# Kernel optimization log

Hardware: AMD Instinct MI355X
Metric: run time of the kernel (lower is better)

The kernel has to match this reference:

```python
import jax, jax.numpy as jnp
import numpy as np
import math

B, S, IN_DIM = 4, 2048, 512
D, H, L, FF = 256, 4, 4, 2048
HD = D // H
EPS = 1e-5


def _pos_encoding(S, D, dtype=jnp.float32):
    pos = jnp.arange(S, dtype=jnp.float32)[:, None]
    div = jnp.exp(jnp.arange(0, D, 2, dtype=jnp.float32) * (-math.log(10000.0) / D))
    pe = jnp.zeros((S, D), dtype=jnp.float32)
    pe = pe.at[:, 0::2].set(jnp.sin(pos * div))
    pe = pe.at[:, 1::2].set(jnp.cos(pos * div))
    return pe.astype(dtype)


def _layernorm(x, w, b):
    mu = jnp.mean(x, axis=-1, keepdims=True)
    var = jnp.var(x, axis=-1, keepdims=True)
    return (x - mu) * jax.lax.rsqrt(var + EPS) * w + b


def setup_inputs() -> dict:
    key = jax.random.key(0)
    ks = jax.random.split(key, 12)
    sc = 0.02
    inp = {
        "x": jax.random.normal(ks[0], (B, S, IN_DIM), dtype=jnp.float32),
        "W_in": jax.random.normal(ks[1], (D, IN_DIM), dtype=jnp.float32) * sc,
        "b_in": jnp.zeros((D,), dtype=jnp.float32),
        "qkv_w": jax.random.normal(ks[2], (L, 3 * D, D), dtype=jnp.float32) * sc,
        "qkv_b": jnp.zeros((L, 3 * D), dtype=jnp.float32),
        "out_w": jax.random.normal(ks[3], (L, D, D), dtype=jnp.float32) * sc,
        "out_b": jnp.zeros((L, D), dtype=jnp.float32),
        "ln1_w": jnp.ones((L, D), dtype=jnp.float32),
        "ln1_b": jnp.zeros((L, D), dtype=jnp.float32),
        "ff1_w": jax.random.normal(ks[4], (L, FF, D), dtype=jnp.float32) * sc,
        "ff1_b": jnp.zeros((L, FF), dtype=jnp.float32),
        "ff2_w": jax.random.normal(ks[5], (L, D, FF), dtype=jnp.float32) * sc,
        "ff2_b": jnp.zeros((L, D), dtype=jnp.float32),
        "ln2_w": jnp.ones((L, D), dtype=jnp.float32),
        "ln2_b": jnp.zeros((L, D), dtype=jnp.float32),
        "W_fc": jax.random.normal(ks[6], (IN_DIM, D), dtype=jnp.float32) * sc,
        "b_fc": jnp.zeros((IN_DIM,), dtype=jnp.float32),
    }
    return inp


def reference(x, W_in, b_in, qkv_w, qkv_b, out_w, out_b, ln1_w, ln1_b,
              ff1_w, ff1_b, ff2_w, ff2_b, ln2_w, ln2_b, W_fc, b_fc):
    # input projection + positional encoding (dropout=0 / eval)
    h = jnp.einsum('bsi,di->bsd', x, W_in) + b_in
    h = h + _pos_encoding(S, D, h.dtype)[None]

    scale = 1.0 / math.sqrt(HD)
    for l in range(L):
        # --- self-attention (unfused: explicit QK^T + softmax + V) ---
        qkv = jnp.einsum('bsd,ed->bse', h, qkv_w[l]) + qkv_b[l]  # [B,S,3D]
        q, k, v = jnp.split(qkv, 3, axis=-1)
        q = q.reshape(B, S, H, HD).transpose(0, 2, 1, 3)  # [B,H,S,HD]
        k = k.reshape(B, S, H, HD).transpose(0, 2, 1, 3)
        v = v.reshape(B, S, H, HD).transpose(0, 2, 1, 3)
        scores = jnp.einsum('bhqd,bhkd->bhqk', q, k) * scale  # [B,H,S,S]
        attn = jax.nn.softmax(scores, axis=-1)
        ctx = jnp.einsum('bhqk,bhkd->bhqd', attn, v)
        ctx = ctx.transpose(0, 2, 1, 3).reshape(B, S, D)
        sa = jnp.einsum('bsd,ed->bse', ctx, out_w[l]) + out_b[l]
        h = _layernorm(h + sa, ln1_w[l], ln1_b[l])  # post-norm
        # --- feed-forward (relu) ---
        ff = jax.nn.relu(jnp.einsum('bsd,fd->bsf', h, ff1_w[l]) + ff1_b[l])
        ff = jnp.einsum('bsf,df->bsd', ff, ff2_w[l]) + ff2_b[l]
        h = _layernorm(h + ff, ln2_w[l], ln2_b[l])

    # final projection from last time step
    return jnp.einsum('bd,od->bo', h[:, -1, :], W_fc) + b_fc  # [B, IN_DIM]
```

## Files before the change

### kernel.cpp

```cpp
#include <hip/hip_runtime.h>
#include <math.h>

#define S_LEN 2048
#define DMODEL 256
#define NHEAD 4
#define HDIM 64
#define NLAYER 4
#define FFDIM 2048
#define INDIM 512
#define BATCH 4
#define NTOK (BATCH * S_LEN)
#define EPSV 1e-5f
#define KSPLIT 4

typedef __attribute__((ext_vector_type(8))) short frag8;
typedef __attribute__((ext_vector_type(4))) float f32x4v;
typedef unsigned short u16;
typedef unsigned int u32;

__device__ __forceinline__ float pe_val(int s, int d) {
    const float c = 0.035977892f;
    float dv = expf(-(float)(d & ~1) * c);
    float arg = (float)s * dv;
    return (d & 1) ? cosf(arg) : sinf(arg);
}

__device__ __forceinline__ u16 f2bf(float f) {
    union { float f; unsigned u; } v; v.f = f;
    unsigned r = v.u + 0x7fffu + ((v.u >> 16) & 1u);
    return (u16)(r >> 16);
}
__device__ __forceinline__ float bf2f(u16 h) {
    union { u32 u; float f; } v; v.u = (u32)h << 16; return v.f;
}
__device__ __forceinline__ u32 pk2bf(float lo, float hi) {
    union { float f; u32 u; } a, b; a.f = lo; b.f = hi;
    return __builtin_amdgcn_perm(b.u, a.u, 0x07060302u);
}
__device__ __forceinline__ void load_lds16(const u16* g, u16* l) {
    __builtin_amdgcn_global_load_lds(
        (const __attribute__((address_space(1))) unsigned int*)g,
        (__attribute__((address_space(3))) unsigned int*)l, 16, 0, 0);
}

__global__ __launch_bounds__(256) void cvt_all(
    const float* __restrict__ x, const float* __restrict__ W_in,
    const float* __restrict__ qkv_w, const float* __restrict__ out_w,
    const float* __restrict__ ff1_w, const float* __restrict__ ff2_w,
    u16* __restrict__ xb, u16* __restrict__ W_in_b,
    u16* __restrict__ qkv_w_b, u16* __restrict__ out_w_b,
    u16* __restrict__ ff1_w_b, u16* __restrict__ ff2_w_b)
{
    const int i = blockIdx.x * 256 + threadIdx.x;
    const float* src; u16* dst; int base;
    if (i < 1048576)      { src = x;     dst = xb;      base = 0; }
    else if (i < 1081344) { src = W_in;  dst = W_in_b;  base = 1048576; }
    else if (i < 1277952) { src = qkv_w; dst = qkv_w_b; base = 1081344; }
    else if (i < 1343488) { src = out_w; dst = out_w_b; base = 1277952; }
    else if (i < 1867776) { src = ff1_w; dst = ff1_w_b; base = 1343488; }
    else                  { src = ff2_w; dst = ff2_w_b; base = 1867776; }
    const int e = (i - base) * 4;
    const float4 v = *(const float4*)(src + e);
    ushort4 o;
    o.x = f2bf(v.x); o.y = f2bf(v.y); o.z = f2bf(v.z); o.w = f2bf(v.w);
    *(ushort4*)(dst + e) = o;
}

template <int MODE>
__global__ __launch_bounds__(256) void gemm_mfma(
    const u16* __restrict__ A, const u16* __restrict__ W,
    const float* __restrict__ bias, u16* __restrict__ Cb,
    int M, int N, int K)
{
    __shared__ __align__(16) u16 As[128 * 32];
    __shared__ __align__(16) u16 Bs[128 * 32];
    const int t = threadIdx.x;
    const int w = t >> 6, lane = t & 63;
    const int col = lane & 15, quad = lane >> 4;
    const int qx = (quad ^ ((col >> 1) & 3)) * 8;
    const int m0 = blockIdx.x * 128, n0 = blockIdx.y * 128;
    const int wm = (w >> 1) * 64, wn = (w & 1) * 64;

    const int r0 = lane >> 2;
    const int kc = ((lane & 3) ^ ((lane >> 3) & 3)) * 8;
    const u16* pA0 = A + (size_t)(m0 + (w * 2 + 0) * 16 + r0) * K + kc;
    const u16* pA1 = A + (size_t)(m0 + (w * 2 + 1) * 16 + r0) * K + kc;
    const u16* pB0 = W + (size_t)(n0 + (w * 2 + 0) * 16 + r0) * K + kc;
    const u16* pB1 = W + (size_t)(n0 + (w * 2 + 1) * 16 + r0) * K + kc;
    u16* lA0 = As + (w * 2 + 0) * 512;
    u16* lA1 = As + (w * 2 + 1) * 512;
    u16* lB0 = Bs + (w * 2 + 0) * 512;
    u16* lB1 = Bs + (w * 2 + 1) * 512;

    f32x4v acc[4][4];
#pragma unroll
    for (int i = 0; i < 4; ++i)
#pragma unroll
        for (int j = 0; j < 4; ++j) acc[i][j] = (f32x4v){0.f, 0.f, 0.f, 0.f};

    for (int kb = 0; kb < K; kb += 32) {
        __syncthreads();
        load_lds16(pA0 + kb, lA0);
        load_lds16(pA1 + kb, lA1);
        load_lds16(pB0 + kb, lB0);
        load_lds16(pB1 + kb, lB1);
        __syncthreads();

        frag8 a[4], b[4];
#pragma unroll
        for (int i = 0; i < 4; ++i)
            a[i] = *(const frag8*)&As[(wm + i * 16 + col) * 32 + qx];
#pragma unroll
        for (int j = 0; j < 4; ++j)
            b[j] = *(const frag8*)&Bs[(wn + j * 16 + col) * 32 + qx];
#pragma unroll
        for (int i = 0; i < 4; ++i)
#pragma unroll
            for (int j = 0; j < 4; ++j)
                acc[i][j] = __builtin_amdgcn_mfma_f32_16x16x32_bf16(
                    a[i], b[j], acc[i][j], 0, 0, 0);
    }

#pragma unroll
    for (int j = 0; j < 4; ++j) {
        const int cn = n0 + wn + j * 16 + col;
        const float bv = bias[cn];
#pragma unroll
        for (int i = 0; i < 4; ++i) {
            const int cmb = m0 + wm + i * 16 + quad * 4;
#pragma unroll
            for (int r = 0; r < 4; ++r) {
                float v = acc[i][j][r] + bv;
                if (MODE == 2) v = fmaxf(v, 0.f);
                Cb[(size_t)(cmb + r) * N + cn] = f2bf(v);
            }
        }
    }
}

template <int MODE>
__global__ __launch_bounds__(256) void gemm64k(
    const u16* __restrict__ A, const u16* __restrict__ W,
    const float* __restrict__ bias, u16* __restrict__ Cb,
    u16* __restrict__ aux, int M, int N, int K)
{
    __shared__ __align__(16) u16 As[64 * 64];
    __shared__ __align__(16) u16 Bs[64 * 64];
    const int t = threadIdx.x;
    const int w = t >> 6, lane = t & 63;
    const int col = lane & 15, quad = lane >> 4;
    const int px0 = ((quad ^ (col & 7))) * 8;
    const int px1 = px0 ^ 32;
    const int m0 = blockIdx.x * 64, n0 = blockIdx.y * 64;
    const int wm = (w >> 1) * 32, wn = (w & 1) * 32;

    const int sr = lane >> 3;
    const int lc = ((lane & 7) ^ sr) * 8;
    const u16* pA0 = A + (size_t)(m0 + w * 16 + sr) * K + lc;
    const u16* pA1 = A + (size_t)(m0 + w * 16 + 8 + sr) * K + lc;
    const u16* pB0 = W + (size_t)(n0 + w * 16 + sr) * K + lc;
    const u16* pB1 = W + (size_t)(n0 + w * 16 + 8 + sr) * K + lc;
    u16* lA0 = As + (w * 16) * 64;
    u16* lA1 = As + (w * 16 + 8) * 64;
    u16* lB0 = Bs + (w * 16) * 64;
    u16* lB1 = Bs + (w * 16 + 8) * 64;

    f32x4v acc[2][2];
#pragma unroll
    for (int i = 0; i < 2; ++i)
#pragma unroll
        for (int j = 0; j < 2; ++j) acc[i][j] = (f32x4v){0.f, 0.f, 0.f, 0.f};

    for (int kb = 0; kb < K; kb += 64) {
        __syncthreads();
        load_lds16(pA0 + kb, lA0);
        load_lds16(pA1 + kb, lA1);
        load_lds16(pB0 + kb, lB0);
        load_lds16(pB1 + kb, lB1);
        __syncthreads();

#pragma unroll
        for (int kh = 0; kh < 2; ++kh) {
            const int px = kh ? px1 : px0;
            frag8 a[2], b[2];
#pragma unroll
            for (int i = 0; i < 2; ++i)
                a[i] = *(const frag8*)&As[(wm + i * 16 + col) * 64 + px];
#pragma unroll
            for (int j = 0; j < 2; ++j)
                b[j] = *(const frag8*)&Bs[(wn + j * 16 + col) * 64 + px];
#pragma unroll
            for (int i = 0; i < 2; ++i)
#pragma unroll
                for (int j = 0; j < 2; ++j)
                    acc[i][j] = __builtin_amdgcn_mfma_f32_16x16x32_bf16(
                        a[i], b[j], acc[i][j], 0, 0, 0);
        }
    }

#pragma unroll
    for (int j = 0; j < 2; ++j) {
        const int cn = n0 + wn + j * 16 + col;
        const float bv = bias[cn];
#pragma unroll
        for (int i = 0; i < 2; ++i) {
            const int cmb = m0 + wm + i * 16 + quad * 4;
            float vv[4];
#pragma unroll
            for (int r = 0; r < 4; ++r) {
                float v = acc[i][j][r] + bv;
                if (MODE == 1) v += pe_val((cmb + r) & (S_LEN - 1), cn);
                if (MODE == 5) v += bf2f(aux[(size_t)(cmb + r) * N + cn]);
                vv[r] = v;
                Cb[(size_t)(cmb + r) * N + cn] = f2bf(v);
            }
            if (MODE == 4 && cn >= 512) {
                const int dg = cn - 512;
                const int bh = (cmb >> 11) * 4 + (dg >> 6);
                uint2 pk;
                pk.x = ((u32)f2bf(vv[1]) << 16) | f2bf(vv[0]);
                pk.y = ((u32)f2bf(vv[3]) << 16) | f2bf(vv[2]);
                *(uint2*)&aux[((size_t)bh * 64 + (dg & 63)) * S_LEN + (cmb & 2047)] = pk;
            }
        }
    }
}

__global__ __launch_bounds__(256) void attn_part(const u16* __restrict__ qkv,
                                                 const u16* __restrict__ vt,
                                                 u16* __restrict__ Opart,
                                                 float* __restrict__ lpart)
{
    __shared__ __align__(16) u16 Ks0[64 * 32], Ks1[64 * 32];
    __shared__ __align__(16) u16 Vt0[64 * 32], Vt1[64 * 32];
    __shared__ __align__(16) u16 Ps[4][2][2][512];

    const int t = threadIdx.x;
    const int w = t >> 6, lane = t & 63;
    const int col = lane & 15, quad = lane >> 4;
    const int sq = (col >> 1) & 3;
    const int qx = (quad ^ sq) * 8;
    const int bh = blockIdx.x, b = bh >> 2, hh = bh & 3;
    const int qt = blockIdx.y, ks = blockIdx.z;

    const float SCL = 0.125f * 1.44269504f;

    frag8 qf[2][2];
#pragma unroll
    for (int qg = 0; qg < 2; ++qg) {
        const int qrow = qt * 128 + w * 32 + qg * 16 + col;
        const u16* qp = qkv + (size_t)(b * S_LEN + qrow) * 768 + hh * HDIM;
        const frag8 r0 = *(const frag8*)(qp + quad * 8);
        const frag8 r1 = *(const frag8*)(qp + 32 + quad * 8);
#pragma unroll
        for (int e = 0; e < 8; ++e) {
            qf[qg][0][e] = (short)f2bf(bf2f((u16)r0[e]) * SCL);
            qf[qg][1][e] = (short)f2bf(bf2f((u16)r1[e]) * SCL);
        }
    }
    frag8 ones;
#pragma unroll
    for (int e = 0; e < 8; ++e) ones[e] = (short)0x3F80;

    f32x4v Oacc[2][4], lacc[2];
#pragma unroll
    for (int qg = 0; qg < 2; ++qg) {
#pragma unroll
        for (int dt = 0; dt < 4; ++dt) Oacc[qg][dt] = (f32x4v){0.f, 0.f, 0.f, 0.f};
        lacc[qg] = (f32x4v){0.f, 0.f, 0.f, 0.f};
    }

    const int srow = w * 16 + (lane >> 2);
    const int sseg = ((lane & 3) ^ ((lane >> 3) & 3)) * 8;
    const int kb0 = ks * (S_LEN / KSPLIT);
    const u16* kbase = qkv + (size_t)(b * S_LEN + kb0 + srow) * 768
                       + 256 + hh * HDIM + sseg;
    const u16* vbase = vt + ((size_t)bh * 64 + srow) * S_LEN + kb0 + sseg;
    u16* lK0 = Ks0 + w * 512;
    u16* lK1 = Ks1 + w * 512;
    u16* lV0 = Vt0 + w * 512;
    u16* lV1 = Vt1 + w * 512;

    for (int kt = 0; kt < S_LEN / KSPLIT / 64; ++kt) {
        __syncthreads();
        const u16* kp = kbase + (size_t)kt * 64 * 768;
        const u16* vp = vbase + kt * 64;
        load_lds16(kp, lK0);
        load_lds16(kp + 32, lK1);
        load_lds16(vp, lV0);
        load_lds16(vp + 32, lV1);
        __syncthreads();

#pragma unroll
        for (int nt = 0; nt < 4; ++nt) {
            const frag8 k0 = *(const frag8*)&Ks0[(nt * 16 + col) * 32 + qx];
            const frag8 k1 = *(const frag8*)&Ks1[(nt * 16 + col) * 32 + qx];
            const int c = (nt & 1) * 2 + (quad >> 1);
            const int poff = col * 32 + ((c ^ sq) * 8) + (quad & 1) * 4;
#pragma unroll
            for (int qg = 0; qg < 2; ++qg) {
                f32x4v s = (f32x4v){0.f, 0.f, 0.f, 0.f};
                s = __builtin_amdgcn_mfma_f32_16x16x32_bf16(k0, qf[qg][0], s, 0, 0, 0);
                s = __builtin_amdgcn_mfma_f32_16x16x32_bf16(k1, qf[qg][1], s, 0, 0, 0);
                const float p0 = __builtin_amdgcn_exp2f(s[0]);
                const float p1 = __builtin_amdgcn_exp2f(s[1]);
                const float p2 = __builtin_amdgcn_exp2f(s[2]);
                const float p3 = __builtin_amdgcn_exp2f(s[3]);
                uint2 pk;
                pk.x = pk2bf(p0, p1);
                pk.y = pk2bf(p2, p3);
                *(uint2*)&Ps[w][qg][nt >> 1][poff] = pk;
            }
        }

        frag8 pf[2][2];
#pragma unroll
        for (int qg = 0; qg < 2; ++qg) {
            pf[qg][0] = *(const frag8*)&Ps[w][qg][0][col * 32 + qx];
            pf[qg][1] = *(const frag8*)&Ps[w][qg][1][col * 32 + qx];
        }
#pragma unroll
        for (int dt = 0; dt < 4; ++dt) {
            const frag8 v0 = *(const frag8*)&Vt0[(dt * 16 + col) * 32 + qx];
            const frag8 v1 = *(const frag8*)&Vt1[(dt * 16 + col) * 32 + qx];
#pragma unroll
            for (int qg = 0; qg < 2; ++qg) {
                Oacc[qg][dt] = __builtin_amdgcn_mfma_f32_16x16x32_bf16(
                    v0, pf[qg][0], Oacc[qg][dt], 0, 0, 0);
                Oacc[qg][dt] = __builtin_amdgcn_mfma_f32_16x16x32_bf16(
                    v1, pf[qg][1], Oacc[qg][dt], 0, 0, 0);
            }
        }
#pragma unroll
        for (int qg = 0; qg < 2; ++qg) {
            lacc[qg] = __builtin_amdgcn_mfma_f32_16x16x32_bf16(
                ones, pf[qg][0], lacc[qg], 0, 0, 0);
            lacc[qg] = __builtin_amdgcn_mfma_f32_16x16x32_bf16(
                ones, pf[qg][1], lacc[qg], 0, 0, 0);
        }
    }

#pragma unroll
    for (int qg = 0; qg < 2; ++qg) {
        const int qrow = qt * 128 + w * 32 + qg * 16 + col;
        u16* op = Opart + (((size_t)ks * 16 + bh) * S_LEN + qrow) * 64;
#pragma unroll
        for (int dt = 0; dt < 4; ++dt) {
            uint2 pk;
            pk.x = pk2bf(Oacc[qg][dt][0], Oacc[qg][dt][1]);
            pk.y = pk2bf(Oacc[qg][dt][2], Oacc[qg][dt][3]);
            *(uint2*)(op + dt * 16 + quad * 4) = pk;
        }
        if (quad == 0)
            lpart[((size_t)ks * 16 + bh) * S_LEN + qrow] = lacc[qg][0];
    }
}

__global__ __launch_bounds__(256) void attn_combine(const u16* __restrict__ Opart,
                                                    const float* __restrict__ lpart,
                                                    u16* __restrict__ ctx)
{
    const int idx = blockIdx.x * 256 + threadIdx.x;
    const int d4 = idx & 15;
    const int q = (idx >> 4) & (S_LEN - 1);
    const int bh = idx >> 15;
    const int b = bh >> 2, hh = bh & 3;

    float o0 = 0.f, o1 = 0.f, o2 = 0.f, o3 = 0.f, l = 0.f;
#pragma unroll
    for (int ks = 0; ks < KSPLIT; ++ks) {
        const ushort4 po = *(const ushort4*)&Opart[
            (((size_t)ks * 16 + bh) * S_LEN + q) * 64 + d4 * 4];
        o0 += bf2f(po.x); o1 += bf2f(po.y);
        o2 += bf2f(po.z); o3 += bf2f(po.w);
        l += lpart[((size_t)ks * 16 + bh) * S_LEN + q];
    }
    const float inv = 1.f / l;
    ushort4 r;
    r.x = f2bf(o0 * inv); r.y = f2bf(o1 * inv);
    r.z = f2bf(o2 * inv); r.w = f2bf(o3 * inv);
    *(ushort4*)&ctx[((size_t)(b * S_LEN + q)) * DMODEL + hh * HDIM + d4 * 4] = r;
}

__global__ __launch_bounds__(256) void ln_only(u16* __restrict__ hb,
                                               const u16* __restrict__ sab,
                                               const float* __restrict__ w,
                                               const float* __restrict__ b)
{
    const int t = blockIdx.x;
    const int d = threadIdx.x;
    const size_t idx = (size_t)t * DMODEL + d;
    const float x = bf2f(sab[idx]);

    float s = x, s2 = x * x;
#pragma unroll
    for (int off = 32; off; off >>= 1) {
        s += __shfl_down(s, off);
        s2 += __shfl_down(s2, off);
    }
    __shared__ float ls[4], ls2[4];
    __shared__ float mu_s, rs_s;
    const int wid = d >> 6, lane = d & 63;
    if (lane == 0) { ls[wid] = s; ls2[wid] = s2; }
    __syncthreads();
    if (d == 0) {
        const float ts = ls[0] + ls[1] + ls[2] + ls[3];
        const float ts2 = ls2[0] + ls2[1] + ls2[2] + ls2[3];
        const float mu = ts * (1.f / DMODEL);
        const float var = ts2 * (1.f / DMODEL) - mu * mu;
        mu_s = mu;
        rs_s = rsqrtf(var + EPSV);
    }
    __syncthreads();
    hb[idx] = f2bf((x - mu_s) * rs_s * w[d] + b[d]);
}

__global__ __launch_bounds__(256) void final_proj(const u16* __restrict__ hb,
                                                  const float* __restrict__ Wfc,
                                                  const float* __restrict__ bfc,
                                                  float* __restrict__ out)
{
    const int idx = blockIdx.x * 256 + threadIdx.x;
    const int b = idx >> 9;
    const int o = idx & 511;
    const u16* hp = hb + (size_t)(b * S_LEN + S_LEN - 1) * DMODEL;
    const float* wp = Wfc + (size_t)o * DMODEL;
    float s = 0.f;
#pragma unroll 4
    for (int d = 0; d < DMODEL; ++d) s += bf2f(hp[d]) * wp[d];
    out[idx] = s + bfc[o];
}

extern "C" void kernel_launch(void* const* d_in, const int* in_sizes, int n_in,
                              void* d_out, int out_size, void* d_ws, size_t ws_size,
                              hipStream_t stream)
{
    const float* x     = (const float*)d_in[0];
    const float* W_in  = (const float*)d_in[1];
    const float* b_in  = (const float*)d_in[2];
    const float* qkv_w = (const float*)d_in[3];
    const float* qkv_b = (const float*)d_in[4];
    const float* out_w = (const float*)d_in[5];
    const float* out_b = (const float*)d_in[6];
    const float* ln1_w = (const float*)d_in[7];
    const float* ln1_b = (const float*)d_in[8];
    const float* ff1_w = (const float*)d_in[9];
    const float* ff1_b = (const float*)d_in[10];
    const float* ff2_w = (const float*)d_in[11];
    const float* ff2_b = (const float*)d_in[12];
    const float* ln2_w = (const float*)d_in[13];
    const float* ln2_b = (const float*)d_in[14];
    const float* W_fc  = (const float*)d_in[15];
    const float* b_fc  = (const float*)d_in[16];
    float* out = (float*)d_out;

    char* p = (char*)d_ws;
    u16* hb    = (u16*)p;  p += (size_t)NTOK * DMODEL * 2;
    u16* sab   = (u16*)p;  p += (size_t)NTOK * DMODEL * 2;
    u16* xb    = (u16*)p;  p += (size_t)NTOK * INDIM * 2;
    u16* qkvb  = (u16*)p;  p += (size_t)NTOK * 768 * 2;
    u16* ctxb  = (u16*)p;  p += (size_t)NTOK * DMODEL * 2;
    u16* ffb   = (u16*)p;  p += (size_t)NTOK * FFDIM * 2;
    u16* vtb   = (u16*)p;  p += (size_t)16 * 64 * S_LEN * 2;
    u16* W_in_b  = (u16*)p; p += (size_t)131072 * 2;
    u16* qkv_w_b = (u16*)p; p += (size_t)786432 * 2;
    u16* out_w_b = (u16*)p; p += (size_t)262144 * 2;
    u16* ff1_w_b = (u16*)p; p += (size_t)2097152 * 2;
    u16* ff2_w_b = (u16*)p; p += (size_t)2097152 * 2;
    if (ws_size < (size_t)82051072) return;

    u16* Opart = ffb;
    float* lpart = (float*)sab;

    cvt_all<<<9344, 256, 0, stream>>>(x, W_in, qkv_w, out_w, ff1_w, ff2_w,
                                      xb, W_in_b, qkv_w_b, out_w_b, ff1_w_b, ff2_w_b);

    gemm64k<1><<<dim3(NTOK / 64, DMODEL / 64), 256, 0, stream>>>(
        xb, W_in_b, b_in, hb, nullptr, NTOK, DMODEL, INDIM);

    for (int l = 0; l < NLAYER; ++l) {
        gemm64k<4><<<dim3(NTOK / 64, 768 / 64), 256, 0, stream>>>(
            hb, qkv_w_b + (size_t)l * 768 * DMODEL, qkv_b + l * 768,
            qkvb, vtb, NTOK, 768, DMODEL);
        attn_part<<<dim3(BATCH * NHEAD, S_LEN / 128, KSPLIT), 256, 0, stream>>>(
            qkvb, vtb, Opart, lpart);
        attn_combine<<<2048, 256, 0, stream>>>(Opart, lpart, ctxb);
        gemm64k<5><<<dim3(NTOK / 64, DMODEL / 64), 256, 0, stream>>>(
            ctxb, out_w_b + (size_t)l * DMODEL * DMODEL, out_b + l * DMODEL,
            sab, hb, NTOK, DMODEL, DMODEL);
        ln_only<<<NTOK, 256, 0, stream>>>(hb, sab, ln1_w + l * DMODEL, ln1_b + l * DMODEL);
        gemm_mfma<2><<<dim3(NTOK / 128, FFDIM / 128), 256, 0, stream>>>(
            hb, ff1_w_b + (size_t)l * FFDIM * DMODEL, ff1_b + l * FFDIM,
            ffb, NTOK, FFDIM, DMODEL);
        gemm64k<5><<<dim3(NTOK / 64, DMODEL / 64), 256, 0, stream>>>(
            ffb, ff2_w_b + (size_t)l * DMODEL * FFDIM, ff2_b + l * DMODEL,
            sab, hb, NTOK, DMODEL, FFDIM);
        ln_only<<<NTOK, 256, 0, stream>>>(hb, sab, ln2_w + l * DMODEL, ln2_b + l * DMODEL);
    }

    final_proj<<<8, 256, 0, stream>>>(hb, W_fc, b_fc, out);
}
```

Baseline: 566.7 us.

## Double-buffer LDS tiles in GEMM and attention kernels to prefetch next tile

Both the 64x64 GEMM kernel and the split-K attention kernel now keep two LDS buffers for their K/A/B (and V) tiles. The next tile is loaded from global memory into the alternate buffer while the MFMA work runs on the current one. This drops one barrier per loop iteration and aims to hide global-load latency behind compute. In exchange each block uses twice the LDS for those tiles, which may reduce occupancy.

After: 574.3 us. No clear change (+1.4%).

```diff
diff --git a/kernel.cpp b/kernel.cpp
--- a/kernel.cpp
+++ b/kernel.cpp
@@ -144,8 +144,8 @@
     const float* __restrict__ bias, u16* __restrict__ Cb,
     u16* __restrict__ aux, int M, int N, int K)
 {
-    __shared__ __align__(16) u16 As[64 * 64];
-    __shared__ __align__(16) u16 Bs[64 * 64];
+    __shared__ __align__(16) u16 As[2][64 * 64];
+    __shared__ __align__(16) u16 Bs[2][64 * 64];
     const int t = threadIdx.x;
     const int w = t >> 6, lane = t & 63;
     const int col = lane & 15, quad = lane >> 4;
@@ -160,10 +160,7 @@
     const u16* pA1 = A + (size_t)(m0 + w * 16 + 8 + sr) * K + lc;
     const u16* pB0 = W + (size_t)(n0 + w * 16 + sr) * K + lc;
     const u16* pB1 = W + (size_t)(n0 + w * 16 + 8 + sr) * K + lc;
-    u16* lA0 = As + (w * 16) * 64;
-    u16* lA1 = As + (w * 16 + 8) * 64;
-    u16* lB0 = Bs + (w * 16) * 64;
-    u16* lB1 = Bs + (w * 16 + 8) * 64;
+    const int o0 = (w * 16) * 64, o1 = (w * 16 + 8) * 64;
 
     f32x4v acc[2][2];
 #pragma unroll
@@ -171,24 +168,32 @@
 #pragma unroll
         for (int j = 0; j < 2; ++j) acc[i][j] = (f32x4v){0.f, 0.f, 0.f, 0.f};
 
-    for (int kb = 0; kb < K; kb += 64) {
+    load_lds16(pA0, &As[0][o0]);
+    load_lds16(pA1, &As[0][o1]);
+    load_lds16(pB0, &Bs[0][o0]);
+    load_lds16(pB1, &Bs[0][o1]);
+
+    const int NIT = K >> 6;
+    for (int it = 0; it < NIT; ++it) {
+        const int cur = it & 1;
         __syncthreads();
-        load_lds16(pA0 + kb, lA0);
-        load_lds16(pA1 + kb, lA1);
-        load_lds16(pB0 + kb, lB0);
-        load_lds16(pB1 + kb, lB1);
-        __syncthreads();
-
+        if (it + 1 < NIT) {
+            const int kb = (it + 1) << 6;
+            load_lds16(pA0 + kb, &As[cur ^ 1][o0]);
+            load_lds16(pA1 + kb, &As[cur ^ 1][o1]);
+            load_lds16(pB0 + kb, &Bs[cur ^ 1][o0]);
+            load_lds16(pB1 + kb, &Bs[cur ^ 1][o1]);
+        }
 #pragma unroll
         for (int kh = 0; kh < 2; ++kh) {
             const int px = kh ? px1 : px0;
             frag8 a[2], b[2];
 #pragma unroll
             for (int i = 0; i < 2; ++i)
-                a[i] = *(const frag8*)&As[(wm + i * 16 + col) * 64 + px];
+                a[i] = *(const frag8*)&As[cur][(wm + i * 16 + col) * 64 + px];
 #pragma unroll
             for (int j = 0; j < 2; ++j)
-                b[j] = *(const frag8*)&Bs[(wn + j * 16 + col) * 64 + px];
+                b[j] = *(const frag8*)&Bs[cur][(wn + j * 16 + col) * 64 + px];
 #pragma unroll
             for (int i = 0; i < 2; ++i)
 #pragma unroll
@@ -231,8 +236,8 @@
                                                  u16* __restrict__ Opart,
                                                  float* __restrict__ lpart)
 {
-    __shared__ __align__(16) u16 Ks0[64 * 32], Ks1[64 * 32];
-    __shared__ __align__(16) u16 Vt0[64 * 32], Vt1[64 * 32];
+    __shared__ __align__(16) u16 Ks[2][2][64 * 32];
+    __shared__ __align__(16) u16 Vt[2][2][64 * 32];
     __shared__ __align__(16) u16 Ps[4][2][2][512];
 
     const int t = threadIdx.x;
@@ -276,25 +281,29 @@
     const u16* kbase = qkv + (size_t)(b * S_LEN + kb0 + srow) * 768
                        + 256 + hh * HDIM + sseg;
     const u16* vbase = vt + ((size_t)bh * 64 + srow) * S_LEN + kb0 + sseg;
-    u16* lK0 = Ks0 + w * 512;
-    u16* lK1 = Ks1 + w * 512;
-    u16* lV0 = Vt0 + w * 512;
-    u16* lV1 = Vt1 + w * 512;
+    const int so = w * 512;
+
+    load_lds16(kbase, &Ks[0][0][so]);
+    load_lds16(kbase + 32, &Ks[0][1][so]);
+    load_lds16(vbase, &Vt[0][0][so]);
+    load_lds16(vbase + 32, &Vt[0][1][so]);
 
     for (int kt = 0; kt < S_LEN / KSPLIT / 64; ++kt) {
+        const int cur = kt & 1;
         __syncthreads();
-        const u16* kp = kbase + (size_t)kt * 64 * 768;
-        const u16* vp = vbase + kt * 64;
-        load_lds16(kp, lK0);
-        load_lds16(kp + 32, lK1);
-        load_lds16(vp, lV0);
-        load_lds16(vp + 32, lV1);
-        __syncthreads();
+        if (kt + 1 < S_LEN / KSPLIT / 64) {
+            const u16* kp = kbase + (size_t)(kt + 1) * 64 * 768;
+            const u16* vp = vbase + (kt + 1) * 64;
+            load_lds16(kp, &Ks[cur ^ 1][0][so]);
+            load_lds16(kp + 32, &Ks[cur ^ 1][1][so]);
+            load_lds16(vp, &Vt[cur ^ 1][0][so]);
+            load_lds16(vp + 32, &Vt[cur ^ 1][1][so]);
+        }
 
 #pragma unroll
         for (int nt = 0; nt < 4; ++nt) {
-            const frag8 k0 = *(const frag8*)&Ks0[(nt * 16 + col) * 32 + qx];
-            const frag8 k1 = *(const frag8*)&Ks1[(nt * 16 + col) * 32 + qx];
+            const frag8 k0 = *(const frag8*)&Ks[cur][0][(nt * 16 + col) * 32 + qx];
+            const frag8 k1 = *(const frag8*)&Ks[cur][1][(nt * 16 + col) * 32 + qx];
             const int c = (nt & 1) * 2 + (quad >> 1);
             const int poff = col * 32 + ((c ^ sq) * 8) + (quad & 1) * 4;
 #pragma unroll
@@ -321,8 +330,8 @@
         }
 #pragma unroll
         for (int dt = 0; dt < 4; ++dt) {
-            const frag8 v0 = *(const frag8*)&Vt0[(dt * 16 + col) * 32 + qx];
-            const frag8 v1 = *(const frag8*)&Vt1[(dt * 16 + col) * 32 + qx];
+            const frag8 v0 = *(const frag8*)&Vt[cur][0][(dt * 16 + col) * 32 + qx];
+            const frag8 v1 = *(const frag8*)&Vt[cur][1][(dt * 16 + col) * 32 + qx];
 #pragma unroll
             for (int qg = 0; qg < 2; ++qg) {
                 Oacc[qg][dt] = __builtin_amdgcn_mfma_f32_16x16x32_bf16(
```

## Fuse attention split-K combine into out-projection GEMM and double-buffer gemm64k

Applied to the files above, without the earlier changes.

Removes the attn_combine kernel. The out-projection GEMM (new MODE 6) now reduces the KSPLIT partial outputs and normalisers while staging its A tile into LDS, so the ctx buffer is never written or re-read. The gemm64k main loop also gains double-buffered LDS with one barrier per iteration, so loads for the next tile are issued before compute on the current one. This cuts a kernel launch and a round trip to global memory, at the cost of doubled LDS and synchronous register-path loads for the combine inside the GEMM. The lpart buffer moves out of sab into its own workspace region.

Measured after the change: 552.6 us. 1.03x faster.

```diff
diff --git a/kernel.cpp b/kernel.cpp
--- a/kernel.cpp
+++ b/kernel.cpp
@@ -142,10 +142,11 @@
 __global__ __launch_bounds__(256) void gemm64k(
     const u16* __restrict__ A, const u16* __restrict__ W,
     const float* __restrict__ bias, u16* __restrict__ Cb,
-    u16* __restrict__ aux, int M, int N, int K)
-{
-    __shared__ __align__(16) u16 As[64 * 64];
-    __shared__ __align__(16) u16 Bs[64 * 64];
+    u16* __restrict__ aux, const float* __restrict__ lp,
+    int M, int N, int K)
+{
+    __shared__ __align__(16) u16 As[2][64 * 64];
+    __shared__ __align__(16) u16 Bs[2][64 * 64];
     const int t = threadIdx.x;
     const int w = t >> 6, lane = t & 63;
     const int col = lane & 15, quad = lane >> 4;
@@ -160,10 +161,7 @@
     const u16* pA1 = A + (size_t)(m0 + w * 16 + 8 + sr) * K + lc;
     const u16* pB0 = W + (size_t)(n0 + w * 16 + sr) * K + lc;
     const u16* pB1 = W + (size_t)(n0 + w * 16 + 8 + sr) * K + lc;
-    u16* lA0 = As + (w * 16) * 64;
-    u16* lA1 = As + (w * 16 + 8) * 64;
-    u16* lB0 = Bs + (w * 16) * 64;
-    u16* lB1 = Bs + (w * 16 + 8) * 64;
+    const int o0 = (w * 16) * 64, o1 = (w * 16 + 8) * 64;
 
     f32x4v acc[2][2];
 #pragma unroll
@@ -171,24 +169,67 @@
 #pragma unroll
         for (int j = 0; j < 2; ++j) acc[i][j] = (f32x4v){0.f, 0.f, 0.f, 0.f};
 
-    for (int kb = 0; kb < K; kb += 64) {
+    auto stageA = [&](int it, int buf) {
+        if (MODE == 6) {
+            const int hh = it;
+#pragma unroll
+            for (int pos = 0; pos < 2; ++pos) {
+                const int m = m0 + w * 16 + pos * 8 + sr;
+                const int q = m & (S_LEN - 1);
+                const int bh = (m >> 11) * 4 + hh;
+                const size_t basei = (((size_t)bh) * S_LEN + q) * 64 + lc;
+                float l = 0.f;
+                float o[8] = {0.f, 0.f, 0.f, 0.f, 0.f, 0.f, 0.f, 0.f};
+#pragma unroll
+                for (int ksx = 0; ksx < KSPLIT; ++ksx) {
+                    const uint4 pv = *(const uint4*)(A + (size_t)ksx * 16 * S_LEN * 64 + basei);
+                    o[0] += bf2f((u16)(pv.x & 0xffff)); o[1] += bf2f((u16)(pv.x >> 16));
+                    o[2] += bf2f((u16)(pv.y & 0xffff)); o[3] += bf2f((u16)(pv.y >> 16));
+                    o[4] += bf2f((u16)(pv.z & 0xffff)); o[5] += bf2f((u16)(pv.z >> 16));
+                    o[6] += bf2f((u16)(pv.w & 0xffff)); o[7] += bf2f((u16)(pv.w >> 16));
+                    l += lp[((size_t)ksx * 16 + bh) * S_LEN + q];
+                }
+                const float inv = 1.f / l;
+                uint4 pk;
+                pk.x = ((u32)f2bf(o[1] * inv) << 16) | f2bf(o[0] * inv);
+                pk.y = ((u32)f2bf(o[3] * inv) << 16) | f2bf(o[2] * inv);
+                pk.z = ((u32)f2bf(o[5] * inv) << 16) | f2bf(o[4] * inv);
+                pk.w = ((u32)f2bf(o[7] * inv) << 16) | f2bf(o[6] * inv);
+                *(uint4*)&As[buf][(pos ? o1 : o0) + lane * 8] = pk;
+            }
+        } else {
+            const int kb = it << 6;
+            load_lds16(pA0 + kb, &As[buf][o0]);
+            load_lds16(pA1 + kb, &As[buf][o1]);
+        }
+    };
+    auto stageB = [&](int it, int buf) {
+        const int kb = it << 6;
+        load_lds16(pB0 + kb, &Bs[buf][o0]);
+        load_lds16(pB1 + kb, &Bs[buf][o1]);
+    };
+
+    stageA(0, 0);
+    stageB(0, 0);
+
+    const int NIT = K >> 6;
+    for (int it = 0; it < NIT; ++it) {
+        const int cur = it & 1;
         __syncthreads();
-        load_lds16(pA0 + kb, lA0);
-        load_lds16(pA1 + kb, lA1);
-        load_lds16(pB0 + kb, lB0);
-        load_lds16(pB1 + kb, lB1);
-        __syncthreads();
-
+        if (it + 1 < NIT) {
+            stageA(it + 1, cur ^ 1);
+            stageB(it + 1, cur ^ 1);
+        }
 #pragma unroll
         for (int kh = 0; kh < 2; ++kh) {
             const int px = kh ? px1 : px0;
             frag8 a[2], b[2];
 #pragma unroll
             for (int i = 0; i < 2; ++i)
-                a[i] = *(const frag8*)&As[(wm + i * 16 + col) * 64 + px];
+                a[i] = *(const frag8*)&As[cur][(wm + i * 16 + col) * 64 + px];
 #pragma unroll
             for (int j = 0; j < 2; ++j)
-                b[j] = *(const frag8*)&Bs[(wn + j * 16 + col) * 64 + px];
+                b[j] = *(const frag8*)&Bs[cur][(wn + j * 16 + col) * 64 + px];
 #pragma unroll
             for (int i = 0; i < 2; ++i)
 #pragma unroll
@@ -210,7 +251,8 @@
             for (int r = 0; r < 4; ++r) {
                 float v = acc[i][j][r] + bv;
                 if (MODE == 1) v += pe_val((cmb + r) & (S_LEN - 1), cn);
-                if (MODE == 5) v += bf2f(aux[(size_t)(cmb + r) * N + cn]);
+                if (MODE == 5 || MODE == 6)
+                    v += bf2f(aux[(size_t)(cmb + r) * N + cn]);
                 vv[r] = v;
                 Cb[(size_t)(cmb + r) * N + cn] = f2bf(v);
             }
@@ -354,32 +396,6 @@
         if (quad == 0)
             lpart[((size_t)ks * 16 + bh) * S_LEN + qrow] = lacc[qg][0];
     }
-}
-
-__global__ __launch_bounds__(256) void attn_combine(const u16* __restrict__ Opart,
-                                                    const float* __restrict__ lpart,
-                                                    u16* __restrict__ ctx)
-{
-    const int idx = blockIdx.x * 256 + threadIdx.x;
-    const int d4 = idx & 15;
-    const int q = (idx >> 4) & (S_LEN - 1);
-    const int bh = idx >> 15;
-    const int b = bh >> 2, hh = bh & 3;
-
-    float o0 = 0.f, o1 = 0.f, o2 = 0.f, o3 = 0.f, l = 0.f;
-#pragma unroll
-    for (int ks = 0; ks < KSPLIT; ++ks) {
-        const ushort4 po = *(const ushort4*)&Opart[
-            (((size_t)ks * 16 + bh) * S_LEN + q) * 64 + d4 * 4];
-        o0 += bf2f(po.x); o1 += bf2f(po.y);
-        o2 += bf2f(po.z); o3 += bf2f(po.w);
-        l += lpart[((size_t)ks * 16 + bh) * S_LEN + q];
-    }
-    const float inv = 1.f / l;
-    ushort4 r;
-    r.x = f2bf(o0 * inv); r.y = f2bf(o1 * inv);
-    r.z = f2bf(o2 * inv); r.w = f2bf(o3 * inv);
-    *(ushort4*)&ctx[((size_t)(b * S_LEN + q)) * DMODEL + hh * HDIM + d4 * 4] = r;
 }
 
 __global__ __launch_bounds__(256) void ln_only(u16* __restrict__ hb,
@@ -459,42 +475,40 @@
     u16* sab   = (u16*)p;  p += (size_t)NTOK * DMODEL * 2;
     u16* xb    = (u16*)p;  p += (size_t)NTOK * INDIM * 2;
     u16* qkvb  = (u16*)p;  p += (size_t)NTOK * 768 * 2;
-    u16* ctxb  = (u16*)p;  p += (size_t)NTOK * DMODEL * 2;
     u16* ffb   = (u16*)p;  p += (size_t)NTOK * FFDIM * 2;
     u16* vtb   = (u16*)p;  p += (size_t)16 * 64 * S_LEN * 2;
+    float* lpart = (float*)p; p += (size_t)KSPLIT * 16 * S_LEN * 4;
     u16* W_in_b  = (u16*)p; p += (size_t)131072 * 2;
     u16* qkv_w_b = (u16*)p; p += (size_t)786432 * 2;
     u16* out_w_b = (u16*)p; p += (size_t)262144 * 2;
     u16* ff1_w_b = (u16*)p; p += (size_t)2097152 * 2;
     u16* ff2_w_b = (u16*)p; p += (size_t)2097152 * 2;
-    if (ws_size < (size_t)82051072) return;
+    if (ws_size < (size_t)78643200) return;
 
     u16* Opart = ffb;
-    float* lpart = (float*)sab;
 
     cvt_all<<<9344, 256, 0, stream>>>(x, W_in, qkv_w, out_w, ff1_w, ff2_w,
                                       xb, W_in_b, qkv_w_b, out_w_b, ff1_w_b, ff2_w_b);
 
     gemm64k<1><<<dim3(NTOK / 64, DMODEL / 64), 256, 0, stream>>>(
-        xb, W_in_b, b_in, hb, nullptr, NTOK, DMODEL, INDIM);
+        xb, W_in_b, b_in, hb, nullptr, nullptr, NTOK, DMODEL, INDIM);
 
     for (int l = 0; l < NLAYER; ++l) {
         gemm64k<4><<<dim3(NTOK / 64, 768 / 64), 256, 0, stream>>>(
             hb, qkv_w_b + (size_t)l * 768 * DMODEL, qkv_b + l * 768,
-            qkvb, vtb, NTOK, 768, DMODEL);
+            qkvb, vtb, nullptr, NTOK, 768, DMODEL);
         attn_part<<<dim3(BATCH * NHEAD, S_LEN / 128, KSPLIT), 256, 0, stream>>>(
             qkvb, vtb, Opart, lpart);
-        attn_combine<<<2048, 256, 0, stream>>>(Opart, lpart, ctxb);
-        gemm64k<5><<<dim3(NTOK / 64, DMODEL / 64), 256, 0, stream>>>(
-            ctxb, out_w_b + (size_t)l * DMODEL * DMODEL, out_b + l * DMODEL,
-            sab, hb, NTOK, DMODEL, DMODEL);
+        gemm64k<6><<<dim3(NTOK / 64, DMODEL / 64), 256, 0, stream>>>(
+            Opart, out_w_b + (size_t)l * DMODEL * DMODEL, out_b + l * DMODEL,
+            sab, hb, lpart, NTOK, DMODEL, DMODEL);
         ln_only<<<NTOK, 256, 0, stream>>>(hb, sab, ln1_w + l * DMODEL, ln1_b + l * DMODEL);
         gemm_mfma<2><<<dim3(NTOK / 128, FFDIM / 128), 256, 0, stream>>>(
             hb, ff1_w_b + (size_t)l * FFDIM * DMODEL, ff1_b + l * FFDIM,
             ffb, NTOK, FFDIM, DMODEL);
         gemm64k<5><<<dim3(NTOK / 64, DMODEL / 64), 256, 0, stream>>>(
             ffb, ff2_w_b + (size_t)l * DMODEL * FFDIM, ff2_b + l * DMODEL,
-            sab, hb, NTOK, DMODEL, FFDIM);
+            sab, hb, nullptr, NTOK, DMODEL, FFDIM);
         ln_only<<<NTOK, 256, 0, stream>>>(hb, sab, ln2_w + l * DMODEL, ln2_b + l * DMODEL);
     }
 
```
